# Optimization experiments

Hardware: AMD Instinct MI355X
Metric: run time of the kernel (lower is better)

The kernel has to match this reference:

```python
import jax, jax.numpy as jnp
import numpy as np

D_IN = 768
D_OUT = 768
NUM_HEADS = 12
HEAD_DIM = D_OUT // NUM_HEADS


def setup_inputs() -> dict:
    key = jax.random.key(0)
    ks = jax.random.split(key, 6)
    s = 0.02
    x = jax.random.normal(ks[0], (2, 4096, D_IN), dtype=jnp.float32)
    w_query = jax.random.normal(ks[1], (D_IN, D_OUT), dtype=jnp.float32) * s
    w_key = jax.random.normal(ks[2], (D_IN, D_OUT), dtype=jnp.float32) * s
    w_value = jax.random.normal(ks[3], (D_IN, D_OUT), dtype=jnp.float32) * s
    w_out = jax.random.normal(ks[4], (D_OUT, D_OUT), dtype=jnp.float32) * s
    b_out = jnp.zeros((D_OUT,), dtype=jnp.float32)
    return {"x": x, "w_query": w_query, "w_key": w_key, "w_value": w_value,
            "w_out": w_out, "b_out": b_out}


def reference(x, w_query, w_key, w_value, w_out, b_out):
    b, n, _ = x.shape
    # projections -> [b, n, h, d]
    q = (x @ w_query).reshape(b, n, NUM_HEADS, HEAD_DIM)
    k = (x @ w_key).reshape(b, n, NUM_HEADS, HEAD_DIM)
    v = (x @ w_value).reshape(b, n, NUM_HEADS, HEAD_DIM)
    # scores [b, h, q, k]
    scores = jnp.einsum('bqhd,bkhd->bhqk', q, k)
    causal = jnp.triu(jnp.ones((n, n), dtype=bool), k=1)  # True above diagonal
    scores = jnp.where(causal, -jnp.inf, scores)
    scale = 1.0 / jnp.sqrt(jnp.asarray(HEAD_DIM, dtype=scores.dtype))
    weights = jax.nn.softmax(scores * scale, axis=-1)
    # dropout p=0.0 -> identity
    ctx = jnp.einsum('bhqk,bkhd->bqhd', weights, v).reshape(b, n, D_OUT)
    return ctx @ w_out + b_out
```

## Files before the change

### kernel.cpp

```cpp
#include <hip/hip_runtime.h>

typedef unsigned short ushort_t;
typedef __bf16 bf16_t;
typedef float floatx4 __attribute__((ext_vector_type(4)));
typedef bf16_t bf16x8 __attribute__((ext_vector_type(8)));
typedef bf16_t bf16x4 __attribute__((ext_vector_type(4)));
typedef short s16x4 __attribute__((ext_vector_type(4)));
typedef float f32x4 __attribute__((ext_vector_type(4)));
typedef unsigned short u16x4 __attribute__((ext_vector_type(4)));
typedef unsigned short u16x8 __attribute__((ext_vector_type(8)));
typedef unsigned int u32x2 __attribute__((ext_vector_type(2)));

#define NTOK 4096
#define NHEAD 12
#define HD 64
#define DMODEL 768
#define NROWS 8192
#define NBH 24

__device__ __forceinline__ ushort_t f2bf(float f) {
  union { float f; unsigned u; } v; v.f = f;
  unsigned u = v.u;
  unsigned r = u + 0x7fffu + ((u >> 16) & 1u);
  return (ushort_t)(r >> 16);
}

__device__ __forceinline__ float bf2f(ushort_t s) {
  union { unsigned u; float f; } v; v.u = (unsigned)s << 16; return v.f;
}

__device__ __forceinline__ void async16(const void* g, void* l) {
  __builtin_amdgcn_global_load_lds(
      (const __attribute__((address_space(1))) void*)g,
      (__attribute__((address_space(3))) void*)l, 16, 0, 0);
}

__device__ __forceinline__ floatx4 mfma16(unsigned a0, unsigned a1,
                                          unsigned b0, unsigned b1, floatx4 c) {
#if defined(__HIP_DEVICE_COMPILE__)
#if __has_builtin(__builtin_amdgcn_mfma_f32_16x16x16_bf16)
  union { unsigned u[2]; bf16x4 v; } A, B;
  A.u[0] = a0; A.u[1] = a1; B.u[0] = b0; B.u[1] = b1;
  return __builtin_amdgcn_mfma_f32_16x16x16_bf16(A.v, B.v, c, 0, 0, 0);
#else
  union { unsigned u[2]; s16x4 v; } A, B;
  A.u[0] = a0; A.u[1] = a1; B.u[0] = b0; B.u[1] = b1;
  return __builtin_amdgcn_mfma_f32_16x16x16bf16_1k(A.v, B.v, c, 0, 0, 0);
#endif
#else
  (void)a0; (void)a1; (void)b0; (void)b1;
  return c;
#endif
}


__global__ __launch_bounds__(256) void transpose_w4(
    const float* __restrict__ s0, const float* __restrict__ s1,
    const float* __restrict__ s2, const float* __restrict__ s3,
    ushort_t* __restrict__ d_qkv, ushort_t* __restrict__ d_o) {
  __shared__ float t[32][33];
  const int m = blockIdx.z;
  const float* src = (m == 0) ? s0 : (m == 1) ? s1 : (m == 2) ? s2 : s3;
  ushort_t* dst = (m < 3) ? (d_qkv + (size_t)m * DMODEL * DMODEL) : d_o;
  const int bi = blockIdx.x, bj = blockIdx.y;
  const int r = threadIdx.x >> 5, c = threadIdx.x & 31;
  for (int p = 0; p < 4; ++p)
    t[r + p * 8][c] = src[(size_t)(bi * 32 + r + p * 8) * DMODEL + bj * 32 + c];
  __syncthreads();
  for (int p = 0; p < 4; ++p)
    dst[(size_t)(bj * 32 + r + p * 8) * DMODEL + bi * 32 + c] = f2bf(t[c][r + p * 8]);
}

__global__ void convert_x(const float* __restrict__ in, ushort_t* __restrict__ out) {
  int idx = blockIdx.x * 256 + threadIdx.x;
  f32x4 v = ((const f32x4*)in)[idx];
  u16x4 o;
  o.x = f2bf(v.x); o.y = f2bf(v.y); o.z = f2bf(v.z); o.w = f2bf(v.w);
  ((u16x4*)out)[idx] = o;
}

__global__ __launch_bounds__(256) void gemm_bt(
    const ushort_t* __restrict__ A, const ushort_t* __restrict__ B, int K, int mode,
    ushort_t* __restrict__ q_ws, ushort_t* __restrict__ k_ws, ushort_t* __restrict__ v_ws,
    float* __restrict__ outF, const float* __restrict__ bias,
    const ushort_t* __restrict__ opart, const float* __restrict__ lpart) {
  __shared__ __align__(16) ushort_t a_lds[128 * 32];
  __shared__ __align__(16) ushort_t b_lds[128 * 32];
  const int tid = threadIdx.x;
  const int w = tid >> 6, lane = tid & 63;
  const int quad = lane >> 4, l16 = lane & 15;
  const int wm = w >> 1, wn = w & 1;
  const size_t row0 = (size_t)blockIdx.x * 128;
  const size_t col0 = (size_t)blockIdx.y * 128;

  const int srow = w * 32 + (lane >> 2);
  const int kbyte = (lane & 3) * 16;
  const char* aG = (const char*)(A + (row0 + srow) * (size_t)K) + kbyte;
  const char* bG = (const char*)(B + (col0 + srow) * (size_t)K) + kbyte;
  const size_t rstep = (size_t)16 * K * 2;
  char* aL = (char*)a_lds + (size_t)(w * 2) * 1024;
  char* bL = (char*)b_lds + (size_t)(w * 2) * 1024;

  floatx4 acc[4][4];
  for (int i = 0; i < 4; ++i)
    for (int j = 0; j < 4; ++j) acc[i][j] = (floatx4){0.f, 0.f, 0.f, 0.f};

  const int nk = K / 32;
  for (int kt = 0; kt < nk; ++kt) {
    const size_t koff = (size_t)kt * 64;
    __syncthreads();
    if (mode == 2) {
      const int col = kt * 32 + (lane & 3) * 8;
      const int h = col >> 6, dd = col & 63;
#pragma unroll
      for (int sl = 0; sl < 2; ++sl) {
        int row = (int)row0 + srow + sl * 16;
        int b = row >> 12, n = row & 4095;
        int bh = b * NHEAD + h;
        size_t i0 = ((size_t)bh * NTOK + n) * HD + dd;
        size_t i1 = i0 + (size_t)NBH * NTOK * HD;
        u16x8 a = *(const u16x8*)&opart[i0];
        u16x8 c = *(const u16x8*)&opart[i1];
        float inv = 1.0f / (lpart[(size_t)bh * NTOK + n] + lpart[(size_t)(NBH + bh) * NTOK + n]);
        u16x8 o;
#pragma unroll
        for (int j = 0; j < 8; ++j) o[j] = f2bf((bf2f(a[j]) + bf2f(c[j])) * inv);
        *(u16x8*)(aL + sl * 1024 + (size_t)lane * 16) = o;
      }
    } else {
      async16(aG + koff, aL);
      async16(aG + koff + rstep, aL + 1024);
    }
    async16(bG + koff, bL);
    async16(bG + koff + rstep, bL + 1024);
    __syncthreads();
    bf16x8 af[4], bfr[4];
    for (int mt = 0; mt < 4; ++mt)
      af[mt] = *(bf16x8*)&a_lds[(wm * 64 + mt * 16 + l16) * 32 + quad * 8];
    for (int nt = 0; nt < 4; ++nt)
      bfr[nt] = *(bf16x8*)&b_lds[(wn * 64 + nt * 16 + l16) * 32 + quad * 8];
    for (int mt = 0; mt < 4; ++mt)
      for (int nt = 0; nt < 4; ++nt)
        acc[mt][nt] = __builtin_amdgcn_mfma_f32_16x16x32_bf16(af[mt], bfr[nt], acc[mt][nt], 0, 0, 0);
  }

  if (mode == 0) {
    const int which = (int)(col0 / DMODEL);
    if (which < 2) {
      ushort_t* dstT = (which == 0) ? q_ws : k_ws;
      const float scale = (which == 0) ? 0.125f * 1.4426950408889634f : 1.0f;
      for (int mt = 0; mt < 4; ++mt) {
        int gr = (int)row0 + wm * 64 + mt * 16 + quad * 4;
        int b = gr >> 12;
        int n0 = gr & 4095;
        for (int nt = 0; nt < 4; ++nt) {
          int gc = (int)col0 + wn * 64 + nt * 16 + l16;
          int cc = gc - which * DMODEL;
          int h = cc >> 6, d = cc & 63;
          size_t base = ((size_t)(b * NHEAD + h) * NTOK + n0) * HD + d;
          for (int r = 0; r < 4; ++r)
            dstT[base + (size_t)r * HD] = f2bf(acc[mt][nt][r] * scale);
        }
      }
    } else {
      for (int mt = 0; mt < 4; ++mt) {
        int gr = (int)row0 + wm * 64 + mt * 16 + quad * 4;
        int b = gr >> 12;
        int n0 = gr & 4095;
        for (int nt = 0; nt < 4; ++nt) {
          int gc = (int)col0 + wn * 64 + nt * 16 + l16;
          int cc = gc - 2 * DMODEL;
          int h = cc >> 6, d = cc & 63;
          u16x4 ov;
          for (int r = 0; r < 4; ++r) ov[r] = f2bf(acc[mt][nt][r]);
          unsigned d0 = ((unsigned*)&ov)[0], d1 = ((unsigned*)&ov)[1];
          unsigned p0 = (unsigned)__shfl_xor((int)d0, 16);
          unsigned p1 = (unsigned)__shfl_xor((int)d1, 16);
          if (!(quad & 1)) {
            u16x8 pk;
            ((unsigned*)&pk)[0] = d0; ((unsigned*)&pk)[1] = d1;
            ((unsigned*)&pk)[2] = p0; ((unsigned*)&pk)[3] = p1;
            *(u16x8*)&v_ws[((size_t)(b * NHEAD + h) * HD + d) * NTOK + n0] = pk;
          }
        }
      }
    }
  } else {
    for (int mt = 0; mt < 4; ++mt) {
      int gr = (int)row0 + wm * 64 + mt * 16 + quad * 4;
      for (int nt = 0; nt < 4; ++nt) {
        int gc = (int)col0 + wn * 64 + nt * 16 + l16;
        float bv = bias[gc];
        for (int r = 0; r < 4; ++r)
          outF[(size_t)(gr + r) * DMODEL + gc] = acc[mt][nt][r] + bv;
      }
    }
  }
}

__global__ __launch_bounds__(256) void attn7(
    const ushort_t* __restrict__ Qh, const ushort_t* __restrict__ Kh,
    const ushort_t* __restrict__ Vt, ushort_t* __restrict__ o_part,
    float* __restrict__ l_part) {
  __shared__ __align__(16) ushort_t k_lds[2][8 * 512];
  __shared__ __align__(16) ushort_t v_lds[2][8 * 512];
  const int tid = threadIdx.x;
  const int w = tid >> 6, lane = tid & 63;
  const int quad = lane >> 4, l16 = lane & 15;
  const int bh = blockIdx.x;
  const int split = blockIdx.z;
  const size_t hbase = (size_t)bh * NTOK * HD;
  const ushort_t* Qb = Qh + hbase;
  const ushort_t* Kb = Kh + hbase;
  const ushort_t* Vb = Vt + hbase;
  const size_t obase = ((size_t)split * NBH + bh) * NTOK * HD;
  const size_t lbase = ((size_t)split * NBH + bh) * NTOK;

  const int vrow = lane >> 3;
  const int vc = lane & 7;
  const int vkoff = ((2 * vc + 16 - 4 * (vrow & 3)) & 15) * 4;
  const int psw = quad + 4 * (l16 & 3);

  for (int phase = 0; phase < 2; ++phase) {
    const int qt = (phase == 0) ? (int)blockIdx.y : 31 - (int)blockIdx.y;
    const int Q0 = qt * 128;
    const int nkt = 2 * qt + 2;
    const int kt_lo = (split == 0) ? 0 : nkt / 2;
    const int nit = nkt / 2;
    __syncthreads();
    char* qstage = (w < 2) ? ((char*)k_lds + 8192 + w * 4096)
                           : ((char*)v_lds + 8192 + (w - 2) * 4096);
#pragma unroll
    for (int i = 0; i < 4; ++i)
      async16(Qb + (size_t)(Q0 + w * 32 + (i >> 1) * 16 + l16) * HD + (i & 1) * 32 + quad * 8,
              qstage + i * 1024);
    {
      const int k0p = kt_lo * 64;
#pragma unroll
      for (int i = 0; i < 2; ++i) {
        int s = w * 2 + i;
        async16(Kb + (size_t)(k0p + (s >> 1) * 16 + l16) * HD + (s & 1) * 32 + quad * 8,
                (char*)k_lds + s * 1024);
        async16(Vb + (size_t)(s * 8 + vrow) * NTOK + k0p + vkoff,
                (char*)v_lds + s * 1024);
      }
    }
    __asm volatile("s_waitcnt vmcnt(0)" ::: "memory");
    bf16x8 qr[2][2];
#pragma unroll
    for (int qf = 0; qf < 2; ++qf)
#pragma unroll
      for (int hh = 0; hh < 2; ++hh)
        qr[qf][hh] = *(const bf16x8*)(qstage + (qf * 2 + hh) * 1024 + lane * 16);

    floatx4 o[2][4];
    float lp[2] = {0.f, 0.f};
#pragma unroll
    for (int qf = 0; qf < 2; ++qf)
#pragma unroll
      for (int dt = 0; dt < 4; ++dt) o[qf][dt] = (floatx4){0.f, 0.f, 0.f, 0.f};

    const int wq0 = Q0 + w * 32;

    for (int it = 0; it < nit; ++it) {
      const int kt = kt_lo + it;
      const int cur = it & 1;
      __syncthreads();
      if (it + 1 < nit) {
        const int k1 = (kt + 1) * 64;
#pragma unroll
        for (int i = 0; i < 2; ++i) {
          int s = w * 2 + i;
          async16(Kb + (size_t)(k1 + (s >> 1) * 16 + l16) * HD + (s & 1) * 32 + quad * 8,
                  (char*)k_lds + (cur ^ 1) * 8192 + s * 1024);
          async16(Vb + (size_t)(s * 8 + vrow) * NTOK + k1 + vkoff,
                  (char*)v_lds + (cur ^ 1) * 8192 + s * 1024);
        }
      }
      const int k0 = kt * 64;
      if (k0 > wq0 + 31) continue;
      const char* kb = (const char*)k_lds + cur * 8192;
      const char* vb = (const char*)v_lds + cur * 8192;
      const bool need_mask = (k0 + 63 > wq0);

#pragma unroll
      for (int g = 0; g < 4; ++g) {
        bf16x8 kf0 = *(const bf16x8*)(kb + (g * 2 + 0) * 1024 + lane * 16);
        bf16x8 kf1 = *(const bf16x8*)(kb + (g * 2 + 1) * 1024 + lane * 16);
        floatx4 z0 = (floatx4){0.f, 0.f, 0.f, 0.f};
        floatx4 z1 = (floatx4){0.f, 0.f, 0.f, 0.f};
        z0 = __builtin_amdgcn_mfma_f32_16x16x32_bf16(kf0, qr[0][0], z0, 0, 0, 0);
        z1 = __builtin_amdgcn_mfma_f32_16x16x32_bf16(kf0, qr[1][0], z1, 0, 0, 0);
        z0 = __builtin_amdgcn_mfma_f32_16x16x32_bf16(kf1, qr[0][1], z0, 0, 0, 0);
        z1 = __builtin_amdgcn_mfma_f32_16x16x32_bf16(kf1, qr[1][1], z1, 0, 0, 0);
        unsigned pa[2][2];
#pragma unroll
        for (int qf = 0; qf < 2; ++qf) {
          floatx4 z = qf ? z1 : z0;
          float p[4];
          const int qg = wq0 + qf * 16 + l16;
#pragma unroll
          for (int r = 0; r < 4; ++r) {
            float e = __builtin_exp2f(z[r]);
            if (need_mask && (k0 + g * 16 + quad * 4 + r > qg)) e = 0.f;
            p[r] = e;
          }
          lp[qf] += (p[0] + p[1]) + (p[2] + p[3]);
          union { float f; unsigned u; } c0, c1, c2, c3;
          c0.f = p[0]; c1.f = p[1]; c2.f = p[2]; c3.f = p[3];
          pa[qf][0] = __builtin_amdgcn_perm(c1.u, c0.u, 0x07060302u);
          pa[qf][1] = __builtin_amdgcn_perm(c3.u, c2.u, 0x07060302u);
        }
        const int pofs = ((g * 4 + psw) & 15) * 8;
#pragma unroll
        for (int dt = 0; dt < 4; ++dt) {
          u32x2 vv = *(const u32x2*)(vb + dt * 2048 + l16 * 128 + pofs);
          o[0][dt] = mfma16(pa[0][0], pa[0][1], vv.x, vv.y, o[0][dt]);
          o[1][dt] = mfma16(pa[1][0], pa[1][1], vv.x, vv.y, o[1][dt]);
        }
      }
    }

#pragma unroll
    for (int qf = 0; qf < 2; ++qf) {
      float lf = lp[qf];
      lf += __shfl_xor(lf, 16);
      lf += __shfl_xor(lf, 32);
#pragma unroll
      for (int r = 0; r < 4; ++r) {
        float lq = __shfl(lf, quad * 4 + r);
        int qg = wq0 + qf * 16 + quad * 4 + r;
        size_t base = obase + (size_t)qg * HD;
#pragma unroll
        for (int dt = 0; dt < 4; ++dt)
          o_part[base + dt * 16 + l16] = f2bf(o[qf][dt][r]);
        if (l16 == 0) l_part[lbase + qg] = lq;
      }
    }
  }
}

extern "C" void kernel_launch(void* const* d_in, const int* in_sizes, int n_in,
                              void* d_out, int out_size, void* d_ws, size_t ws_size,
                              hipStream_t stream) {
  const float* x  = (const float*)d_in[0];
  const float* wq = (const float*)d_in[1];
  const float* wk = (const float*)d_in[2];
  const float* wv = (const float*)d_in[3];
  const float* wo = (const float*)d_in[4];
  const float* bo = (const float*)d_in[5];
  float* out = (float*)d_out;

  ushort_t* ws = (ushort_t*)d_ws;
  ushort_t* wqkvT = ws;
  ushort_t* woutT = wqkvT + 2304 * 768;
  ushort_t* xbf   = woutT + 768 * 768;
  ushort_t* qh    = xbf + (size_t)NROWS * DMODEL;
  ushort_t* kh    = qh + (size_t)NBH * NTOK * HD;
  ushort_t* vt    = kh + (size_t)NBH * NTOK * HD;
  ushort_t* opart = vt + (size_t)NBH * NTOK * HD;
  float*    lpart = (float*)(opart + (size_t)2 * NBH * NTOK * HD);

  transpose_w4<<<dim3(24, 24, 4), 256, 0, stream>>>(wq, wk, wv, wo, wqkvT, woutT);
  convert_x<<<6144, 256, 0, stream>>>(x, xbf);

  gemm_bt<<<dim3(64, 18), 256, 0, stream>>>(xbf, wqkvT, DMODEL, 0,
                                            qh, kh, vt, nullptr, nullptr, nullptr, nullptr);
  attn7<<<dim3(24, 16, 2), 256, 0, stream>>>(qh, kh, vt, opart, lpart);
  gemm_bt<<<dim3(64, 6), 256, 0, stream>>>(opart, woutT, DMODEL, 2,
                                           nullptr, nullptr, nullptr, out, bo, opart, lpart);
}
```

Before: 282.8 us.

## Hoist K/V LDS fragment loads and re-swizzle V tile layout in attention

Loads all eight K fragments and all sixteen V fragments from LDS at the top of each key tile, before the MFMA chain, so LDS latency overlaps with compute instead of being interleaved per group. Changes the V tile swizzle (vkoff and the read offset pattern) to an 8-way 16-byte scheme intended to reduce bank conflicts. Adds a launch-bounds occupancy hint of 3 blocks per CU, which caps registers while the hoisting raises register pressure, so spills are possible.

```diff
diff --git a/kernel.cpp b/kernel.cpp
--- a/kernel.cpp
+++ b/kernel.cpp
@@ -198,7 +198,7 @@
   }
 }
 
-__global__ __launch_bounds__(256) void attn7(
+__global__ __launch_bounds__(256, 3) void attn8(
     const ushort_t* __restrict__ Qh, const ushort_t* __restrict__ Kh,
     const ushort_t* __restrict__ Vt, ushort_t* __restrict__ o_part,
     float* __restrict__ l_part) {
@@ -218,8 +218,9 @@
 
   const int vrow = lane >> 3;
   const int vc = lane & 7;
-  const int vkoff = ((2 * vc + 16 - 4 * (vrow & 3)) & 15) * 4;
-  const int psw = quad + 4 * (l16 & 3);
+  const int vkoff = ((vc - vrow) & 7) * 8;
+  const int vrbase = l16 * 128 + (quad & 1) * 8;
+  const int padd = (quad >> 1) + (l16 & 7);
 
   for (int phase = 0; phase < 2; ++phase) {
     const int qt = (phase == 0) ? (int)blockIdx.y : 31 - (int)blockIdx.y;
@@ -283,16 +284,27 @@
       const char* vb = (const char*)v_lds + cur * 8192;
       const bool need_mask = (k0 + 63 > wq0);
 
+      bf16x8 kf[8];
+#pragma unroll
+      for (int j = 0; j < 8; ++j)
+        kf[j] = *(const bf16x8*)(kb + j * 1024 + lane * 16);
+      u32x2 vv[4][4];
 #pragma unroll
       for (int g = 0; g < 4; ++g) {
-        bf16x8 kf0 = *(const bf16x8*)(kb + (g * 2 + 0) * 1024 + lane * 16);
-        bf16x8 kf1 = *(const bf16x8*)(kb + (g * 2 + 1) * 1024 + lane * 16);
+        const int pofs = ((g * 2 + padd) & 7) * 16;
+#pragma unroll
+        for (int dt = 0; dt < 4; ++dt)
+          vv[g][dt] = *(const u32x2*)(vb + dt * 2048 + vrbase + pofs);
+      }
+
+#pragma unroll
+      for (int g = 0; g < 4; ++g) {
         floatx4 z0 = (floatx4){0.f, 0.f, 0.f, 0.f};
         floatx4 z1 = (floatx4){0.f, 0.f, 0.f, 0.f};
-        z0 = __builtin_amdgcn_mfma_f32_16x16x32_bf16(kf0, qr[0][0], z0, 0, 0, 0);
-        z1 = __builtin_amdgcn_mfma_f32_16x16x32_bf16(kf0, qr[1][0], z1, 0, 0, 0);
-        z0 = __builtin_amdgcn_mfma_f32_16x16x32_bf16(kf1, qr[0][1], z0, 0, 0, 0);
-        z1 = __builtin_amdgcn_mfma_f32_16x16x32_bf16(kf1, qr[1][1], z1, 0, 0, 0);
+        z0 = __builtin_amdgcn_mfma_f32_16x16x32_bf16(kf[g * 2 + 0], qr[0][0], z0, 0, 0, 0);
+        z1 = __builtin_amdgcn_mfma_f32_16x16x32_bf16(kf[g * 2 + 0], qr[1][0], z1, 0, 0, 0);
+        z0 = __builtin_amdgcn_mfma_f32_16x16x32_bf16(kf[g * 2 + 1], qr[0][1], z0, 0, 0, 0);
+        z1 = __builtin_amdgcn_mfma_f32_16x16x32_bf16(kf[g * 2 + 1], qr[1][1], z1, 0, 0, 0);
         unsigned pa[2][2];
 #pragma unroll
         for (int qf = 0; qf < 2; ++qf) {
@@ -311,12 +323,10 @@
           pa[qf][0] = __builtin_amdgcn_perm(c1.u, c0.u, 0x07060302u);
           pa[qf][1] = __builtin_amdgcn_perm(c3.u, c2.u, 0x07060302u);
         }
-        const int pofs = ((g * 4 + psw) & 15) * 8;
 #pragma unroll
         for (int dt = 0; dt < 4; ++dt) {
-          u32x2 vv = *(const u32x2*)(vb + dt * 2048 + l16 * 128 + pofs);
-          o[0][dt] = mfma16(pa[0][0], pa[0][1], vv.x, vv.y, o[0][dt]);
-          o[1][dt] = mfma16(pa[1][0], pa[1][1], vv.x, vv.y, o[1][dt]);
+          o[0][dt] = mfma16(pa[0][0], pa[0][1], vv[g][dt].x, vv[g][dt].y, o[0][dt]);
+          o[1][dt] = mfma16(pa[1][0], pa[1][1], vv[g][dt].x, vv[g][dt].y, o[1][dt]);
         }
       }
     }
@@ -366,7 +376,7 @@
 
   gemm_bt<<<dim3(64, 18), 256, 0, stream>>>(xbf, wqkvT, DMODEL, 0,
                                             qh, kh, vt, nullptr, nullptr, nullptr, nullptr);
-  attn7<<<dim3(24, 16, 2), 256, 0, stream>>>(qh, kh, vt, opart, lpart);
+  attn8<<<dim3(24, 16, 2), 256, 0, stream>>>(qh, kh, vt, opart, lpart);
   gemm_bt<<<dim3(64, 6), 256, 0, stream>>>(opart, woutT, DMODEL, 2,
                                            nullptr, nullptr, nullptr, out, bo, opart, lpart);
 }
```

New measurement: 269.9 us. 1.05x faster.
